# Kernel tuning notes

Measured on AMD Instinct MI355X. Metric: run time of the kernel, lower is better.

The kernel has to match this reference:

```python
import jax, jax.numpy as jnp
import numpy as np

N = 16384  # n_nodes
D = 64     # feature dim


def setup_inputs() -> dict:
    key = jax.random.key(0)
    kx, ka = jax.random.split(key)
    x = jax.random.normal(kx, (N, D), dtype=jnp.float32)
    # original code only tests adj[idx] == 1, so 0/1 int entries are faithful
    adj = jax.random.randint(ka, (N, N), 0, 2, dtype=jnp.int32)
    return {"x": x, "adj": adj}


def reference(x, adj):
    # GraphPool: for each node, sum its own feature vector plus the feature
    # vectors of all neighbors j with adj[i, j] == 1.
    # Vectorized: out = adj @ x + x  (dense binary SpMM + self term).
    a = (adj == 1).astype(x.dtype)  # [N, N]
    return jnp.matmul(a, x) + x     # [N, D]
```

## Files before the change

kernel.cpp:

```cpp
#include <hip/hip_runtime.h>

#define NN 16384
#define DD 64

typedef _Float16 f16x8 __attribute__((ext_vector_type(8)));
typedef short    s16x8 __attribute__((ext_vector_type(8)));
typedef float    f32x4 __attribute__((ext_vector_type(4)));
typedef int      i32x4 __attribute__((ext_vector_type(4)));
typedef int      i32x2 __attribute__((ext_vector_type(2)));
typedef unsigned u32;
typedef unsigned long long u64;

__global__ __launch_bounds__(256) void prep_x(const float* __restrict__ x,
                                              _Float16* __restrict__ ws) {
    __shared__ float sx[32][65];
    const int tid = threadIdx.x;
    const int t   = blockIdx.x;
    {
        int r  = tid >> 3;
        int c8 = (tid & 7) * 8;
        const float* src = x + ((size_t)t * 32 + r) * DD + c8;
        f32x4 a = *(const f32x4*)src;
        f32x4 b = *(const f32x4*)(src + 4);
#pragma unroll
        for (int j = 0; j < 4; ++j) { sx[r][c8 + j] = a[j]; sx[r][c8 + 4 + j] = b[j]; }
    }
    __syncthreads();
    const int l = tid & 63;
    const int c = tid >> 6;
    const int q = l >> 4;
    const int m = l & 15;
    f16x8 v;
#pragma unroll
    for (int j = 0; j < 8; ++j)
        v[j] = (_Float16)sx[q * 8 + j][c * 16 + m];
    *(f16x8*)(ws + (((size_t)t * 256 + c * 64 + l) * 8)) = v;
}

__global__ __launch_bounds__(256, 3) void graphpool_gemm(const int* __restrict__ adj,
                                                         const _Float16* __restrict__ xs,
                                                         float* __restrict__ part) {
    __shared__ _Float16 sB[2][8192];
    __shared__ u32      sA[2][256];

    const int tid = threadIdx.x;
    const int w   = tid >> 6;
    const int l   = tid & 63;
    const int q   = l >> 4;
    const int m   = l & 15;

    const int rb    = blockIdx.x >> 1;
    const int kq    = blockIdx.x & 1;
    const int row16 = rb * 64 + w * 16;
    constexpr int KH  = NN / 2;
    constexpr int NCH = KH / 128;

    const int* abase = adj + (size_t)row16 * NN + (size_t)kq * KH;

    f32x4 acc[4];
#pragma unroll
    for (int c = 0; c < 4; ++c) acc[c] = (f32x4){0.f, 0.f, 0.f, 0.f};

    i32x2 areg[16];
    f16x8 sreg[4];

    auto loadAdj = [&](int n) {
#pragma unroll
        for (int rr = 0; rr < 16; ++rr) {
            const i32x2* p = (const i32x2*)(abase + (size_t)rr * NN + n * 128);
            areg[rr] = p[l];
        }
    };
    auto packA = [&](int buf) {
        u32 mine = 0;
#pragma unroll
        for (int rr = 0; rr < 16; ++rr) {
            u64 b0 = __ballot(areg[rr].x != 0);
            u64 b1 = __ballot(areg[rr].y != 0);
            u32 lo0 = (u32)b0, hi0 = (u32)(b0 >> 32);
            u32 lo1 = (u32)b1, hi1 = (u32)(b1 >> 32);
            u32 sa  = (l & 1) ? hi0 : lo0;
            u32 sb  = (l & 1) ? hi1 : lo1;
            u32 sel = (l & 2) ? sb : sa;
            if ((l >> 2) == rr) mine = sel;
        }
        sA[buf][w * 64 + l] = mine;
    };
    auto stageRead = [&](int n) {
        const f16x8* src = (const f16x8*)xs + ((size_t)kq * NCH + n) * 1024;
#pragma unroll
        for (int p = 0; p < 4; ++p) sreg[p] = src[p * 256 + tid];
    };
    auto stageWrite = [&](int buf) {
        f16x8* dst = (f16x8*)sB[buf];
#pragma unroll
        for (int p = 0; p < 4; ++p) dst[p * 256 + tid] = sreg[p];
    };

    loadAdj(0);
    stageRead(0);
    packA(0);
    stageWrite(0);
    __syncthreads();

    for (int n = 0; n < NCH; ++n) {
        const int buf = n & 1;
        const bool pf = (n + 1 < NCH);
        if (pf) { loadAdj(n + 1); stageRead(n + 1); }

        i32x4 rowAi = *(const i32x4*)&sA[buf][(w * 16 + m) * 4];
#pragma unroll
        for (int s = 0; s < 4; ++s) {
            const u32 bq = 16 * (s & 1) + 4 * q;
            const u32 dE = (u32)rowAi[s >> 1];
            const u32 dO = (u32)rowAi[2 + (s >> 1)];
            s16x8 ai;
#pragma unroll
            for (int j = 0; j < 8; ++j) {
                u32 d = (j & 1) ? dO : dE;
                ai[j] = ((d >> (bq + (j >> 1))) & 1u) ? (short)0x3C00 : (short)0;
            }
            f16x8 af = __builtin_bit_cast(f16x8, ai);
#pragma unroll
            for (int c = 0; c < 4; ++c) {
                f16x8 bf = *(const f16x8*)&sB[buf][((s * 4 + c) * 64 + l) * 8];
                acc[c] = __builtin_amdgcn_mfma_f32_16x16x32_f16(af, bf, acc[c], 0, 0, 0);
            }
        }

        if (pf) { packA(buf ^ 1); stageWrite(buf ^ 1); }
        __syncthreads();
    }

    float* po = part + (size_t)kq * NN * DD;
#pragma unroll
    for (int c = 0; c < 4; ++c) {
#pragma unroll
        for (int r = 0; r < 4; ++r) {
            size_t off = (size_t)(row16 + q * 4 + r) * DD + c * 16 + m;
            po[off] = acc[c][r];
        }
    }
}

__global__ __launch_bounds__(256) void reduce_add(const float* __restrict__ part,
                                                  const float* __restrict__ x,
                                                  float* __restrict__ out) {
    size_t i = (size_t)blockIdx.x * 256 + threadIdx.x;
    f32x4 v = ((const f32x4*)x)[i];
    v += ((const f32x4*)part)[i];
    v += ((const f32x4*)(part + (size_t)NN * DD))[i];
    ((f32x4*)out)[i] = v;
}

__global__ void graphpool_fallback(const int* __restrict__ adj,
                                   const float* __restrict__ x,
                                   float* __restrict__ out) {
    int i = blockIdx.x;
    int d = threadIdx.x;
    float acc = x[(size_t)i * DD + d];
    const int* row = adj + (size_t)i * NN;
    for (int j = 0; j < NN; ++j)
        if (row[j]) acc += x[(size_t)j * DD + d];
    out[(size_t)i * DD + d] = acc;
}

extern "C" void kernel_launch(void* const* d_in, const int* in_sizes, int n_in,
                              void* d_out, int out_size, void* d_ws, size_t ws_size,
                              hipStream_t stream) {
    const float* x   = (const float*)d_in[0];
    const int*   adj = (const int*)d_in[1];
    float*       out = (float*)d_out;

    const size_t xs_bytes   = (size_t)NN * DD * sizeof(_Float16);
    const size_t part_bytes = (size_t)2 * NN * DD * sizeof(float);
    if (ws_size >= xs_bytes + part_bytes) {
        _Float16* xs   = (_Float16*)d_ws;
        float*    part = (float*)((char*)d_ws + xs_bytes);
        prep_x<<<512, 256, 0, stream>>>(x, xs);
        graphpool_gemm<<<512, 256, 0, stream>>>(adj, xs, part);
        reduce_add<<<1024, 256, 0, stream>>>(part, x, out);
    } else {
        graphpool_fallback<<<NN, 64, 0, stream>>>(adj, x, out);
    }
}
```

Measured before the change: 1.388 ms.

## Split K 32 ways, preload x slice to LDS, exchange masks via bpermute

Raises the K-split from 2 to 32, so the grid grows from 512 to 8192 blocks. Each block loads its whole 512-column fp16 x slice (64 KB) into LDS once, which removes the per-chunk LDS double buffer and the block-wide barriers. Adjacency rows are double-buffered in registers two chunks ahead, and the packed bit masks move between lanes with ds_bpermute instead of through shared memory. The cost is 32 partial outputs (128 MB of writes plus a 32-way reduce) and lower occupancy from the larger LDS footprint, all to get more parallelism for streaming the 1 GB adjacency matrix.

```diff
diff --git a/kernel.cpp b/kernel.cpp
--- a/kernel.cpp
+++ b/kernel.cpp
@@ -2,6 +2,9 @@
 
 #define NN 16384
 #define DD 64
+#define SPLIT 32
+#define KQ (NN / SPLIT)
+#define NCH (KQ / 128)
 
 typedef _Float16 f16x8 __attribute__((ext_vector_type(8)));
 typedef short    s16x8 __attribute__((ext_vector_type(8)));
@@ -37,11 +40,10 @@
     *(f16x8*)(ws + (((size_t)t * 256 + c * 64 + l) * 8)) = v;
 }
 
-__global__ __launch_bounds__(256, 3) void graphpool_gemm(const int* __restrict__ adj,
+__global__ __launch_bounds__(256, 2) void graphpool_gemm(const int* __restrict__ adj,
                                                          const _Float16* __restrict__ xs,
                                                          float* __restrict__ part) {
-    __shared__ _Float16 sB[2][8192];
-    __shared__ u32      sA[2][256];
+    __shared__ _Float16 sB[NCH][8192];
 
     const int tid = threadIdx.x;
     const int w   = tid >> 6;
@@ -49,66 +51,58 @@
     const int q   = l >> 4;
     const int m   = l & 15;
 
-    const int rb    = blockIdx.x >> 1;
-    const int kq    = blockIdx.x & 1;
+    const int rb    = blockIdx.x >> 5;
+    const int kq    = blockIdx.x & 31;
     const int row16 = rb * 64 + w * 16;
-    constexpr int KH  = NN / 2;
-    constexpr int NCH = KH / 128;
 
-    const int* abase = adj + (size_t)row16 * NN + (size_t)kq * KH;
+#pragma unroll
+    for (int n = 0; n < NCH; ++n) {
+        const f16x8* src = (const f16x8*)xs + ((size_t)(kq * NCH + n)) * 1024;
+        f16x8 t0 = src[tid], t1 = src[256 + tid], t2 = src[512 + tid], t3 = src[768 + tid];
+        f16x8* dst = (f16x8*)sB[n];
+        dst[tid] = t0; dst[256 + tid] = t1; dst[512 + tid] = t2; dst[768 + tid] = t3;
+    }
+    __syncthreads();
+
+    const int* abase = adj + (size_t)row16 * NN + (size_t)kq * KQ;
 
     f32x4 acc[4];
 #pragma unroll
     for (int c = 0; c < 4; ++c) acc[c] = (f32x4){0.f, 0.f, 0.f, 0.f};
 
-    i32x2 areg[16];
-    f16x8 sreg[4];
+    i32x2 areg[2][16];
 
-    auto loadAdj = [&](int n) {
+    auto loadAdj = [&](int n, int buf) {
 #pragma unroll
-        for (int rr = 0; rr < 16; ++rr) {
-            const i32x2* p = (const i32x2*)(abase + (size_t)rr * NN + n * 128);
-            areg[rr] = p[l];
-        }
+        for (int rr = 0; rr < 16; ++rr)
+            areg[buf][rr] = ((const i32x2*)(abase + (size_t)rr * NN + n * 128))[l];
     };
-    auto packA = [&](int buf) {
+
+    loadAdj(0, 0);
+    loadAdj(1, 1);
+
+#pragma unroll
+    for (int n = 0; n < NCH; ++n) {
+        const int buf = n & 1;
+
         u32 mine = 0;
 #pragma unroll
         for (int rr = 0; rr < 16; ++rr) {
-            u64 b0 = __ballot(areg[rr].x != 0);
-            u64 b1 = __ballot(areg[rr].y != 0);
-            u32 lo0 = (u32)b0, hi0 = (u32)(b0 >> 32);
-            u32 lo1 = (u32)b1, hi1 = (u32)(b1 >> 32);
-            u32 sa  = (l & 1) ? hi0 : lo0;
-            u32 sb  = (l & 1) ? hi1 : lo1;
+            u64 b0 = __ballot(areg[buf][rr].x != 0);
+            u64 b1 = __ballot(areg[buf][rr].y != 0);
+            u32 sa = (l & 1) ? (u32)(b0 >> 32) : (u32)b0;
+            u32 sb = (l & 1) ? (u32)(b1 >> 32) : (u32)b1;
             u32 sel = (l & 2) ? sb : sa;
             if ((l >> 2) == rr) mine = sel;
         }
-        sA[buf][w * 64 + l] = mine;
-    };
-    auto stageRead = [&](int n) {
-        const f16x8* src = (const f16x8*)xs + ((size_t)kq * NCH + n) * 1024;
+
+        if (n + 2 < NCH) loadAdj(n + 2, buf);
+
+        i32x4 rowAi;
 #pragma unroll
-        for (int p = 0; p < 4; ++p) sreg[p] = src[p * 256 + tid];
-    };
-    auto stageWrite = [&](int buf) {
-        f16x8* dst = (f16x8*)sB[buf];
-#pragma unroll
-        for (int p = 0; p < 4; ++p) dst[p * 256 + tid] = sreg[p];
-    };
+        for (int d = 0; d < 4; ++d)
+            rowAi[d] = __builtin_amdgcn_ds_bpermute(((m << 2) | d) << 2, (int)mine);
 
-    loadAdj(0);
-    stageRead(0);
-    packA(0);
-    stageWrite(0);
-    __syncthreads();
-
-    for (int n = 0; n < NCH; ++n) {
-        const int buf = n & 1;
-        const bool pf = (n + 1 < NCH);
-        if (pf) { loadAdj(n + 1); stageRead(n + 1); }
-
-        i32x4 rowAi = *(const i32x4*)&sA[buf][(w * 16 + m) * 4];
 #pragma unroll
         for (int s = 0; s < 4; ++s) {
             const u32 bq = 16 * (s & 1) + 4 * q;
@@ -117,19 +111,16 @@
             s16x8 ai;
 #pragma unroll
             for (int j = 0; j < 8; ++j) {
-                u32 d = (j & 1) ? dO : dE;
-                ai[j] = ((d >> (bq + (j >> 1))) & 1u) ? (short)0x3C00 : (short)0;
+                u32 dd = (j & 1) ? dO : dE;
+                ai[j] = ((dd >> (bq + (j >> 1))) & 1u) ? (short)0x3C00 : (short)0;
             }
             f16x8 af = __builtin_bit_cast(f16x8, ai);
 #pragma unroll
             for (int c = 0; c < 4; ++c) {
-                f16x8 bf = *(const f16x8*)&sB[buf][((s * 4 + c) * 64 + l) * 8];
+                f16x8 bf = *(const f16x8*)&sB[n][((s * 4 + c) * 64 + l) * 8];
                 acc[c] = __builtin_amdgcn_mfma_f32_16x16x32_f16(af, bf, acc[c], 0, 0, 0);
             }
         }
-
-        if (pf) { packA(buf ^ 1); stageWrite(buf ^ 1); }
-        __syncthreads();
     }
 
     float* po = part + (size_t)kq * NN * DD;
@@ -148,8 +139,9 @@
                                                   float* __restrict__ out) {
     size_t i = (size_t)blockIdx.x * 256 + threadIdx.x;
     f32x4 v = ((const f32x4*)x)[i];
-    v += ((const f32x4*)part)[i];
-    v += ((const f32x4*)(part + (size_t)NN * DD))[i];
+#pragma unroll
+    for (int g = 0; g < SPLIT; ++g)
+        v += ((const f32x4*)(part + (size_t)g * NN * DD))[i];
     ((f32x4*)out)[i] = v;
 }
 
@@ -173,12 +165,12 @@
     float*       out = (float*)d_out;
 
     const size_t xs_bytes   = (size_t)NN * DD * sizeof(_Float16);
-    const size_t part_bytes = (size_t)2 * NN * DD * sizeof(float);
+    const size_t part_bytes = (size_t)SPLIT * NN * DD * sizeof(float);
     if (ws_size >= xs_bytes + part_bytes) {
         _Float16* xs   = (_Float16*)d_ws;
         float*    part = (float*)((char*)d_ws + xs_bytes);
         prep_x<<<512, 256, 0, stream>>>(x, xs);
-        graphpool_gemm<<<512, 256, 0, stream>>>(adj, xs, part);
+        graphpool_gemm<<<256 * SPLIT, 256, 0, stream>>>(adj, xs, part);
         reduce_add<<<1024, 256, 0, stream>>>(part, x, out);
     } else {
         graphpool_fallback<<<NN, 64, 0, stream>>>(adj, x, out);
```

Measured after the change: 1.363 ms. Within noise of the previous version (-1.8%).
